# Optimization experiments

Measured on AMD Instinct MI355X. Metric: run time of the kernel, lower is better.

Reference implementation:

```python
import jax, jax.numpy as jnp
import numpy as np

D, H, HD, E, TOPK, F = 2048, 16, 128, 64, 8, 1024
EPS = 1e-5
THETA = 10000.0
ATTN_SCALE = 0.08838834764831845  # 1/sqrt(128)
B, S = 1, 1024


def setup_inputs() -> dict:
    key = jax.random.key(0)
    ks = jax.random.split(key, 16)
    w = 0.02  # init scale so activations stay O(1)
    return {
        "x": jax.random.normal(ks[0], (B, S, D), jnp.float32),
        "input_ln_w": jnp.ones((D,), jnp.float32),
        "q_w": jax.random.normal(ks[1], (D, D), jnp.float32) * w,
        "q_norm_w": jnp.ones((D,), jnp.float32),
        "k_w": jax.random.normal(ks[2], (D, D), jnp.float32) * w,
        "k_norm_w": jnp.ones((D,), jnp.float32),
        "v_w": jax.random.normal(ks[3], (D, D), jnp.float32) * w,
        "o_w": jax.random.normal(ks[4], (D, D), jnp.float32) * w,
        "post_ln_w": jnp.ones((D,), jnp.float32),
        "router_w": jax.random.normal(ks[5], (E, D), jnp.float32) * w,
        "gate_w": jax.random.normal(ks[6], (E, F, D), jnp.float32) * w,
        "up_w": jax.random.normal(ks[7], (E, F, D), jnp.float32) * w,
        "down_w": jax.random.normal(ks[8], (E, D, F), jnp.float32) * w,
    }


def _rmsnorm(h, w):
    return h * jax.lax.rsqrt(jnp.mean(h * h, axis=-1, keepdims=True) + EPS) * w


def _rope(t, cos, sin):
    # t: [B,H,S,HD]; HF rotate_half convention
    t1, t2 = t[..., : HD // 2], t[..., HD // 2 :]
    return jnp.concatenate([t1 * cos - t2 * sin, t2 * cos + t1 * sin], axis=-1)


def reference(x, input_ln_w, q_w, q_norm_w, k_w, k_norm_w, v_w, o_w,
              post_ln_w, router_w, gate_w, up_w, down_w):
    b, s, _ = x.shape
    # ---- attention ----
    xn = _rmsnorm(x, input_ln_w)
    q = _rmsnorm(xn @ q_w.T, q_norm_w)  # full-width q_norm before head split
    k = _rmsnorm(xn @ k_w.T, k_norm_w)
    v = xn @ v_w.T
    q = q.reshape(b, s, H, HD).transpose(0, 2, 1, 3)  # [B,H,S,HD]
    k = k.reshape(b, s, H, HD).transpose(0, 2, 1, 3)
    v = v.reshape(b, s, H, HD).transpose(0, 2, 1, 3)
    pos = jnp.arange(s, dtype=jnp.float32)
    inv_freq = 1.0 / (THETA ** (jnp.arange(0, HD, 2, dtype=jnp.float32) / HD))
    ang = pos[:, None] * inv_freq[None, :]  # [S,HD/2]
    cos, sin = jnp.cos(ang), jnp.sin(ang)
    q, k = _rope(q, cos, sin), _rope(k, cos, sin)
    scores = jnp.einsum("bhqd,bhkd->bhqk", q, k) * ATTN_SCALE
    causal = jnp.tril(jnp.ones((s, s), bool))
    scores = jnp.where(causal, scores, jnp.finfo(scores.dtype).min)
    probs = jax.nn.softmax(scores, axis=-1)
    ctx = jnp.einsum("bhqk,bhkd->bhqd", probs, v)
    attn = ctx.transpose(0, 2, 1, 3).reshape(b, s, D) @ o_w.T
    x = x + attn
    # ---- MoE (top-8 of 64, softmax weights, not renormalized) ----
    h = _rmsnorm(x, post_ln_w)
    logits = h @ router_w.T  # [B,S,E]
    rprobs = jax.nn.softmax(logits.astype(jnp.float32), axis=-1)
    topw, topi = jax.lax.top_k(rprobs, TOPK)  # [B,S,K]
    onehot = jax.nn.one_hot(topi, E, dtype=rprobs.dtype)  # [B,S,K,E]
    wfull = jnp.einsum("bske,bsk->bse", onehot, topw).astype(h.dtype)  # [B,S,E]
    moe = jnp.zeros_like(h)
    for e in range(E):  # fixed expert loop (not a data-dim loop)
        g = h @ gate_w[e].T            # [B,S,F]
        u = h @ up_w[e].T
        y = (jax.nn.silu(g) * u) @ down_w[e].T  # [B,S,D]
        moe = moe + wfull[..., e:e + 1] * y
    return x + moe
```

## Files before the change

### kernel.cpp

```cpp
#include <hip/hip_runtime.h>
#include <hip/hip_bf16.h>
#include <math.h>

#define NTOK 1024
#define DIM 2048
#define NH 16
#define HDIM 128
#define NE 64
#define NTOP 8
#define FF 1024
#define EPSI 1e-5f
#define ASCALE 0.08838834764831845f

typedef __attribute__((ext_vector_type(8))) short bh8;
typedef __attribute__((ext_vector_type(4))) float f4;

static __device__ __forceinline__ ushort f2bf(float f) {
  return __builtin_bit_cast(ushort, __float2bfloat16(f));
}

__global__ __launch_bounds__(256) void k_rmsnorm(const float* __restrict__ in,
                                                 const float* __restrict__ w,
                                                 float* __restrict__ out,
                                                 ushort* __restrict__ outb) {
  int row = blockIdx.x, tid = threadIdx.x;
  const float* r = in + (size_t)row * DIM;
  float ss = 0.f;
  for (int i = tid; i < DIM; i += 256) { float v = r[i]; ss += v * v; }
#pragma unroll
  for (int o = 1; o < 64; o <<= 1) ss += __shfl_xor(ss, o, 64);
  __shared__ float red[4];
  if ((tid & 63) == 0) red[tid >> 6] = ss;
  __syncthreads();
  float rstd = rsqrtf((red[0] + red[1] + red[2] + red[3]) / (float)DIM + EPSI);
  if (out) {
    float* o_ = out + (size_t)row * DIM;
    ushort* ob = outb + (size_t)row * DIM;
    for (int i = tid; i < DIM; i += 256) {
      float v = r[i] * rstd * w[i];
      o_[i] = v; ob[i] = f2bf(v);
    }
  } else {
    ushort* ob = outb + (size_t)row * DIM;
    for (int i = tid; i < DIM; i += 256) ob[i] = f2bf(r[i] * rstd * w[i]);
  }
}

template <int KDIM>
static __device__ __forceinline__ void mm_tile(
    const ushort* __restrict__ Ap0, const ushort* __restrict__ Ap1,
    const float* __restrict__ Wp, ushort (*As)[40], ushort (*Bs)[40],
    int ar0, int ac0, int wrow, int wcol, int wr, int wc, int fr, int fq,
    f4 (&acc)[4][4]) {
  bh8 aR0 = *(const bh8*)Ap0;
  bh8 aR1 = *(const bh8*)Ap1;
  f4 wR[4];
#pragma unroll
  for (int i = 0; i < 4; i++) wR[i] = *(const f4*)(Wp + (size_t)(32 * i) * KDIM);
  for (int k0 = 0; k0 < KDIM; k0 += 32) {
    __syncthreads();
    *(bh8*)&As[ar0][ac0] = aR0;
    *(bh8*)&As[ar0 + 64][ac0] = aR1;
#pragma unroll
    for (int i = 0; i < 4; i++) {
      ushort4 t = make_ushort4(f2bf(wR[i].x), f2bf(wR[i].y), f2bf(wR[i].z), f2bf(wR[i].w));
      *(ushort4*)&Bs[wrow + 32 * i][wcol] = t;
    }
    __syncthreads();
    if (k0 + 32 < KDIM) {
      aR0 = *(const bh8*)(Ap0 + k0 + 32);
      aR1 = *(const bh8*)(Ap1 + k0 + 32);
#pragma unroll
      for (int i = 0; i < 4; i++) wR[i] = *(const f4*)(Wp + (size_t)(32 * i) * KDIM + k0 + 32);
    }
    bh8 af[4], bf_[4];
#pragma unroll
    for (int m = 0; m < 4; m++) af[m] = *(const bh8*)&As[wr * 64 + m * 16 + fr][fq * 8];
#pragma unroll
    for (int n = 0; n < 4; n++) bf_[n] = *(const bh8*)&Bs[wc * 64 + n * 16 + fr][fq * 8];
#pragma unroll
    for (int m = 0; m < 4; m++)
#pragma unroll
      for (int n = 0; n < 4; n++)
        acc[m][n] = __builtin_amdgcn_mfma_f32_16x16x32_bf16(af[m], bf_[n], acc[m][n], 0, 0, 0);
  }
}

__global__ __launch_bounds__(256) void k_gemm_qkv(
    const ushort* __restrict__ A, const float* __restrict__ Wq,
    const float* __restrict__ Wk, const float* __restrict__ Wv,
    float* __restrict__ Cq, float* __restrict__ Ck, float* __restrict__ Cv) {
  __shared__ ushort As[128][40], Bs[128][40];
  int tid = threadIdx.x;
  int m0 = blockIdx.y * 128;
  int ng = blockIdx.x * 128;
  int wsel = ng >> 11, n0 = ng & 2047;
  const float* W = wsel == 0 ? Wq : wsel == 1 ? Wk : Wv;
  float* C = wsel == 0 ? Cq : wsel == 1 ? Ck : Cv;
  int lane = tid & 63, wid = tid >> 6;
  int wr = wid >> 1, wc = wid & 1, fr = lane & 15, fq = lane >> 4;
  int ar0 = tid >> 2, ac0 = (tid & 3) * 8;
  int wrow = tid >> 3, wcol = (tid & 7) * 4;
  const ushort* Ap0 = A + (size_t)(m0 + ar0) * DIM + ac0;
  const ushort* Ap1 = Ap0 + (size_t)64 * DIM;
  const float* Wp = W + (size_t)(n0 + wrow) * DIM + wcol;
  f4 acc[4][4];
  f4 z = {0.f, 0.f, 0.f, 0.f};
#pragma unroll
  for (int m = 0; m < 4; m++)
#pragma unroll
    for (int n = 0; n < 4; n++) acc[m][n] = z;
  mm_tile<DIM>(Ap0, Ap1, Wp, As, Bs, ar0, ac0, wrow, wcol, wr, wc, fr, fq, acc);
#pragma unroll
  for (int m = 0; m < 4; m++)
#pragma unroll
    for (int n = 0; n < 4; n++) {
      int row = m0 + wr * 64 + m * 16 + fq * 4;
      int col = n0 + wc * 64 + n * 16 + fr;
#pragma unroll
      for (int r = 0; r < 4; r++) C[(size_t)(row + r) * DIM + col] = acc[m][n][r];
    }
}

__global__ __launch_bounds__(256) void k_gemm_o(
    const ushort* __restrict__ A, const float* __restrict__ W,
    const float* __restrict__ R, float* __restrict__ C) {
  __shared__ ushort As[128][40], Bs[128][40];
  int tid = threadIdx.x;
  int m0 = blockIdx.y * 128, n0 = blockIdx.x * 128;
  int lane = tid & 63, wid = tid >> 6;
  int wr = wid >> 1, wc = wid & 1, fr = lane & 15, fq = lane >> 4;
  int ar0 = tid >> 2, ac0 = (tid & 3) * 8;
  int wrow = tid >> 3, wcol = (tid & 7) * 4;
  const ushort* Ap0 = A + (size_t)(m0 + ar0) * DIM + ac0;
  const ushort* Ap1 = Ap0 + (size_t)64 * DIM;
  const float* Wp = W + (size_t)(n0 + wrow) * DIM + wcol;
  f4 acc[4][4];
  f4 z = {0.f, 0.f, 0.f, 0.f};
#pragma unroll
  for (int m = 0; m < 4; m++)
#pragma unroll
    for (int n = 0; n < 4; n++) acc[m][n] = z;
  mm_tile<DIM>(Ap0, Ap1, Wp, As, Bs, ar0, ac0, wrow, wcol, wr, wc, fr, fq, acc);
#pragma unroll
  for (int m = 0; m < 4; m++)
#pragma unroll
    for (int n = 0; n < 4; n++) {
      int row = m0 + wr * 64 + m * 16 + fq * 4;
      int col = n0 + wc * 64 + n * 16 + fr;
#pragma unroll
      for (int r = 0; r < 4; r++) {
        size_t o = (size_t)(row + r) * DIM + col;
        C[o] = acc[m][n][r] + R[o];
      }
    }
}

__global__ __launch_bounds__(256) void k_qknorm_rope(
    const float* __restrict__ q, const float* __restrict__ k,
    const float* __restrict__ v, const float* __restrict__ qw,
    const float* __restrict__ kw, float* __restrict__ qr,
    float* __restrict__ kr, float* __restrict__ vr) {
  int s = blockIdx.x, tid = threadIdx.x;
  __shared__ float cst[64], snt[64];
  if (tid < 64) {
    float inv = powf(10000.f, -(float)tid / 64.f);
    float ang = (float)s * inv;
    cst[tid] = cosf(ang);
    snt[tid] = sinf(ang);
  }
  const float* qrow = q + (size_t)s * DIM;
  const float* krow = k + (size_t)s * DIM;
  const float* vrow = v + (size_t)s * DIM;
  float sq = 0.f, sk = 0.f;
  for (int i = tid; i < DIM; i += 256) {
    float a = qrow[i]; sq += a * a;
    float b = krow[i]; sk += b * b;
  }
#pragma unroll
  for (int o = 1; o < 64; o <<= 1) {
    sq += __shfl_xor(sq, o, 64);
    sk += __shfl_xor(sk, o, 64);
  }
  __shared__ float red[8];
  if ((tid & 63) == 0) { red[tid >> 6] = sq; red[4 + (tid >> 6)] = sk; }
  __syncthreads();
  float rq = rsqrtf((red[0] + red[1] + red[2] + red[3]) / (float)DIM + EPSI);
  float rk = rsqrtf((red[4] + red[5] + red[6] + red[7]) / (float)DIM + EPSI);
  for (int idx = tid; idx < NH * 64; idx += 256) {
    int hh = idx >> 6, i = idx & 63;
    float c = cst[i], sn = snt[i];
    int b = hh * HDIM + i;
    float q1 = qrow[b] * rq * qw[b];
    float q2 = qrow[b + 64] * rq * qw[b + 64];
    float k1 = krow[b] * rk * kw[b];
    float k2 = krow[b + 64] * rk * kw[b + 64];
    size_t ob = ((size_t)hh * NTOK + s) * HDIM + i;
    qr[ob] = q1 * c - q2 * sn;
    qr[ob + 64] = q2 * c + q1 * sn;
    kr[ob] = k1 * c - k2 * sn;
    kr[ob + 64] = k2 * c + k1 * sn;
  }
  for (int idx = tid; idx < DIM; idx += 256) {
    int hh = idx >> 7, d = idx & 127;
    vr[((size_t)hh * NTOK + s) * HDIM + d] = vrow[idx];
  }
}

__global__ __launch_bounds__(256) void k_attn(const float* __restrict__ qr,
                                              const float* __restrict__ kr,
                                              const float* __restrict__ vr,
                                              ushort* __restrict__ ctx) {
  int h = blockIdx.y, qt = blockIdx.x;
  __shared__ __align__(16) float Ks[64][HDIM];
  __shared__ __align__(16) float Vs[64][HDIM];
  int tid = threadIdx.x;
  int ql = tid >> 2, sub = tid & 3;
  int qg = qt * 64 + ql;
  const float* qrow = qr + ((size_t)h * NTOK + qg) * HDIM + sub * 32;
  float4 q4[8], acc[8];
#pragma unroll
  for (int i = 0; i < 8; i++) {
    q4[i] = *(const float4*)(qrow + i * 4);
    acc[i] = make_float4(0.f, 0.f, 0.f, 0.f);
  }
  float m = -1e30f, l = 0.f;
  for (int kt = 0; kt <= qt; kt++) {
    __syncthreads();
    const float4* kg = (const float4*)(kr + ((size_t)h * NTOK + kt * 64) * HDIM);
    const float4* vg = (const float4*)(vr + ((size_t)h * NTOK + kt * 64) * HDIM);
#pragma unroll
    for (int i = 0; i < 8; i++) {
      int e4 = tid + i * 256;
      ((float4*)Ks)[e4] = kg[e4];
      ((float4*)Vs)[e4] = vg[e4];
    }
    __syncthreads();
    int jmax = min(64, qg - kt * 64 + 1);
    for (int j = 0; j < jmax; j++) {
      const float4* kj = (const float4*)&Ks[j][sub * 32];
      float sc = 0.f;
#pragma unroll
      for (int i = 0; i < 8; i++) {
        float4 kv = kj[i];
        sc += q4[i].x * kv.x + q4[i].y * kv.y + q4[i].z * kv.z + q4[i].w * kv.w;
      }
      sc += __shfl_xor(sc, 1, 64);
      sc += __shfl_xor(sc, 2, 64);
      sc *= ASCALE;
      float mn = fmaxf(m, sc);
      float al = __expf(m - mn);
      float p = __expf(sc - mn);
      l = l * al + p;
      const float4* vj = (const float4*)&Vs[j][sub * 32];
#pragma unroll
      for (int i = 0; i < 8; i++) {
        float4 vv = vj[i];
        acc[i].x = acc[i].x * al + p * vv.x;
        acc[i].y = acc[i].y * al + p * vv.y;
        acc[i].z = acc[i].z * al + p * vv.z;
        acc[i].w = acc[i].w * al + p * vv.w;
      }
      m = mn;
    }
  }
  float invl = 1.f / l;
  ushort* crow = ctx + (size_t)qg * DIM + h * HDIM + sub * 32;
#pragma unroll
  for (int i = 0; i < 8; i++) {
    float4 o = acc[i];
    ushort4 t = make_ushort4(f2bf(o.x * invl), f2bf(o.y * invl),
                             f2bf(o.z * invl), f2bf(o.w * invl));
    *(ushort4*)(crow + i * 4) = t;
  }
}

__global__ void k_zero_counts(int* counts) {
  if (threadIdx.x < NE) counts[threadIdx.x] = 0;
}

__global__ __launch_bounds__(256) void k_router(const float* __restrict__ h,
                                                const float* __restrict__ rw,
                                                float* __restrict__ topw,
                                                int* __restrict__ lists,
                                                int* __restrict__ counts) {
  int s = blockIdx.x, tid = threadIdx.x;
  int e = tid >> 2, sub = tid & 3;
  const float* hrow = h + (size_t)s * DIM;
  const float* wrow = rw + (size_t)e * DIM;
  float p = 0.f;
  for (int i = sub * 4; i < DIM; i += 16) {
    float4 hv = *(const float4*)(hrow + i);
    float4 wv = *(const float4*)(wrow + i);
    p += hv.x * wv.x + hv.y * wv.y + hv.z * wv.z + hv.w * wv.w;
  }
  p += __shfl_xor(p, 1, 64);
  p += __shfl_xor(p, 2, 64);
  __shared__ float probs[NE];
  if (sub == 0) probs[e] = p;
  __syncthreads();
  if (tid == 0) {
    float mx = -1e30f;
    for (int i = 0; i < NE; i++) mx = fmaxf(mx, probs[i]);
    float sum = 0.f;
    for (int i = 0; i < NE; i++) { probs[i] = __expf(probs[i] - mx); sum += probs[i]; }
    float inv = 1.f / sum;
    for (int kk = 0; kk < NTOP; kk++) {
      float best = -1.f; int bi = 0;
      for (int i = 0; i < NE; i++)
        if (probs[i] > best) { best = probs[i]; bi = i; }
      topw[s * NTOP + kk] = best * inv;
      probs[bi] = -1.f;
      int slot = atomicAdd(&counts[bi], 1);
      lists[bi * NTOK + slot] = s * NTOP + kk;
    }
  }
}

__global__ __launch_bounds__(256) void k_moe_gate_up(
    const ushort* __restrict__ hb, const float* __restrict__ gate,
    const float* __restrict__ up, const int* __restrict__ lists,
    const int* __restrict__ counts, ushort* __restrict__ act) {
  int e = blockIdx.z;
  int nt = counts[e];
  int m0 = blockIdx.y * 128;
  if (m0 >= nt) return;
  __shared__ ushort As[128][40], Gs[128][40], Us[128][40];
  int f0 = blockIdx.x * 128;
  int tid = threadIdx.x;
  int lane = tid & 63, wid = tid >> 6;
  int wr = wid >> 1, wc = wid & 1, fr = lane & 15, fq = lane >> 4;
  int ar0 = tid >> 2, ac0 = (tid & 3) * 8;
  int wrow = tid >> 3, wcol = (tid & 7) * 4;
  int r0 = m0 + ar0, r1 = r0 + 64;
  int g0 = lists[e * NTOK + (r0 < nt ? r0 : nt - 1)];
  int g1 = lists[e * NTOK + (r1 < nt ? r1 : nt - 1)];
  const ushort* Ap0 = hb + (size_t)(g0 >> 3) * DIM + ac0;
  const ushort* Ap1 = hb + (size_t)(g1 >> 3) * DIM + ac0;
  const float* Gp = gate + ((size_t)e * FF + f0 + wrow) * DIM + wcol;
  const float* Up = up + ((size_t)e * FF + f0 + wrow) * DIM + wcol;
  f4 ag[4][4], au[4][4];
  f4 z = {0.f, 0.f, 0.f, 0.f};
#pragma unroll
  for (int m = 0; m < 4; m++)
#pragma unroll
    for (int n = 0; n < 4; n++) { ag[m][n] = z; au[m][n] = z; }
  bh8 aR0 = *(const bh8*)Ap0;
  bh8 aR1 = *(const bh8*)Ap1;
  f4 gR[4], uR[4];
#pragma unroll
  for (int i = 0; i < 4; i++) {
    gR[i] = *(const f4*)(Gp + (size_t)(32 * i) * DIM);
    uR[i] = *(const f4*)(Up + (size_t)(32 * i) * DIM);
  }
  for (int k0 = 0; k0 < DIM; k0 += 32) {
    __syncthreads();
    *(bh8*)&As[ar0][ac0] = aR0;
    *(bh8*)&As[ar0 + 64][ac0] = aR1;
#pragma unroll
    for (int i = 0; i < 4; i++) {
      ushort4 tg = make_ushort4(f2bf(gR[i].x), f2bf(gR[i].y), f2bf(gR[i].z), f2bf(gR[i].w));
      *(ushort4*)&Gs[wrow + 32 * i][wcol] = tg;
      ushort4 tu = make_ushort4(f2bf(uR[i].x), f2bf(uR[i].y), f2bf(uR[i].z), f2bf(uR[i].w));
      *(ushort4*)&Us[wrow + 32 * i][wcol] = tu;
    }
    __syncthreads();
    if (k0 + 32 < DIM) {
      aR0 = *(const bh8*)(Ap0 + k0 + 32);
      aR1 = *(const bh8*)(Ap1 + k0 + 32);
#pragma unroll
      for (int i = 0; i < 4; i++) {
        gR[i] = *(const f4*)(Gp + (size_t)(32 * i) * DIM + k0 + 32);
        uR[i] = *(const f4*)(Up + (size_t)(32 * i) * DIM + k0 + 32);
      }
    }
    bh8 af[4], bg_[4], bu_[4];
#pragma unroll
    for (int m = 0; m < 4; m++) af[m] = *(const bh8*)&As[wr * 64 + m * 16 + fr][fq * 8];
#pragma unroll
    for (int n = 0; n < 4; n++) {
      bg_[n] = *(const bh8*)&Gs[wc * 64 + n * 16 + fr][fq * 8];
      bu_[n] = *(const bh8*)&Us[wc * 64 + n * 16 + fr][fq * 8];
    }
#pragma unroll
    for (int m = 0; m < 4; m++)
#pragma unroll
      for (int n = 0; n < 4; n++) {
        ag[m][n] = __builtin_amdgcn_mfma_f32_16x16x32_bf16(af[m], bg_[n], ag[m][n], 0, 0, 0);
        au[m][n] = __builtin_amdgcn_mfma_f32_16x16x32_bf16(af[m], bu_[n], au[m][n], 0, 0, 0);
      }
  }
#pragma unroll
  for (int m = 0; m < 4; m++) {
#pragma unroll
    for (int r = 0; r < 4; r++) {
      int mrow = m0 + wr * 64 + m * 16 + fq * 4 + r;
      if (mrow < nt) {
        int gg = lists[e * NTOK + mrow];
        ushort* arow = act + (size_t)gg * FF + f0 + wc * 64 + fr;
#pragma unroll
        for (int n = 0; n < 4; n++) {
          float gv = ag[m][n][r], uv = au[m][n][r];
          float sv = gv / (1.f + __expf(-gv)) * uv;
          arow[n * 16] = f2bf(sv);
        }
      }
    }
  }
}

__global__ __launch_bounds__(256) void k_moe_down(
    const ushort* __restrict__ act, const float* __restrict__ down,
    const int* __restrict__ lists, const int* __restrict__ counts,
    const float* __restrict__ topw, float* __restrict__ out) {
  int e = blockIdx.z;
  int nt = counts[e];
  int m0 = blockIdx.y * 128;
  if (m0 >= nt) return;
  __shared__ ushort As[128][40], Bs[128][40];
  int n0 = blockIdx.x * 128;
  int tid = threadIdx.x;
  int lane = tid & 63, wid = tid >> 6;
  int wr = wid >> 1, wc = wid & 1, fr = lane & 15, fq = lane >> 4;
  int ar0 = tid >> 2, ac0 = (tid & 3) * 8;
  int wrow = tid >> 3, wcol = (tid & 7) * 4;
  int r0 = m0 + ar0, r1 = r0 + 64;
  int g0 = lists[e * NTOK + (r0 < nt ? r0 : nt - 1)];
  int g1 = lists[e * NTOK + (r1 < nt ? r1 : nt - 1)];
  const ushort* Ap0 = act + (size_t)g0 * FF + ac0;
  const ushort* Ap1 = act + (size_t)g1 * FF + ac0;
  const float* Wp = down + ((size_t)e * DIM + n0 + wrow) * FF + wcol;
  f4 acc[4][4];
  f4 z = {0.f, 0.f, 0.f, 0.f};
#pragma unroll
  for (int m = 0; m < 4; m++)
#pragma unroll
    for (int n = 0; n < 4; n++) acc[m][n] = z;
  mm_tile<FF>(Ap0, Ap1, Wp, As, Bs, ar0, ac0, wrow, wcol, wr, wc, fr, fq, acc);
#pragma unroll
  for (int m = 0; m < 4; m++) {
#pragma unroll
    for (int r = 0; r < 4; r++) {
      int mrow = m0 + wr * 64 + m * 16 + fq * 4 + r;
      if (mrow < nt) {
        int gg = lists[e * NTOK + mrow];
        int s = gg >> 3;
        float wgt = topw[gg];
        float* orow = out + (size_t)s * DIM + n0 + wc * 64 + fr;
#pragma unroll
        for (int n = 0; n < 4; n++) atomicAdd(&orow[n * 16], wgt * acc[m][n][r]);
      }
    }
  }
}

extern "C" void kernel_launch(void* const* d_in, const int* in_sizes, int n_in,
                              void* d_out, int out_size, void* d_ws, size_t ws_size,
                              hipStream_t stream) {
  const float* x   = (const float*)d_in[0];
  const float* iln = (const float*)d_in[1];
  const float* qw  = (const float*)d_in[2];
  const float* qnw = (const float*)d_in[3];
  const float* kw  = (const float*)d_in[4];
  const float* knw = (const float*)d_in[5];
  const float* vw  = (const float*)d_in[6];
  const float* ow  = (const float*)d_in[7];
  const float* pln = (const float*)d_in[8];
  const float* rw  = (const float*)d_in[9];
  const float* gw  = (const float*)d_in[10];
  const float* uw  = (const float*)d_in[11];
  const float* dw  = (const float*)d_in[12];
  float* out = (float*)d_out;
  float* ws = (float*)d_ws;

  const size_t M2 = (size_t)NTOK * DIM;
  float* qb = ws + 0 * M2;
  float* kb = ws + 1 * M2;
  float* vb = ws + 2 * M2;
  float* qr = ws + 3 * M2;
  float* kr = ws + 4 * M2;
  float* vr = ws + 5 * M2;
  ushort* xnb = (ushort*)(ws + 6 * M2);
  ushort* hb  = xnb + M2;
  ushort* ctxb = (ushort*)kb;
  float* topw = kb + M2 / 2;
  int* lists = (int*)(topw + NTOK * NTOP);
  int* counts = lists + NE * NTOK;
  float* h = qb;
  ushort* act = (ushort*)vb;

  k_rmsnorm<<<NTOK, 256, 0, stream>>>(x, iln, nullptr, xnb);
  k_gemm_qkv<<<dim3(48, 8), 256, 0, stream>>>(xnb, qw, kw, vw, qb, kb, vb);
  k_qknorm_rope<<<NTOK, 256, 0, stream>>>(qb, kb, vb, qnw, knw, qr, kr, vr);
  k_attn<<<dim3(NTOK / 64, NH), 256, 0, stream>>>(qr, kr, vr, ctxb);
  k_gemm_o<<<dim3(16, 8), 256, 0, stream>>>(ctxb, ow, x, out);
  k_rmsnorm<<<NTOK, 256, 0, stream>>>(out, pln, h, hb);
  k_zero_counts<<<1, 64, 0, stream>>>(counts);
  k_router<<<NTOK, 256, 0, stream>>>(h, rw, topw, lists, counts);
  k_moe_gate_up<<<dim3(FF / 128, NTOK / 128, NE), 256, 0, stream>>>(hb, gw, uw, lists, counts, act);
  k_moe_down<<<dim3(DIM / 128, NTOK / 128, NE), 256, 0, stream>>>(act, dw, lists, counts, topw, out);
}
```

Baseline: 2.489 ms.

## Rewrite MoE expert GEMMs as LDS-free register-direct MFMA with expert-fastest block ordering

The MoE gate/up and down kernels no longer stage tiles in shared memory and no longer synchronise. Each wave now loads its 16-row weight slice straight from global memory, converts it to bf16 in registers, and runs MFMA against 8 gathered token rows. The tile shrinks to 128 tokens by 64 outputs. The grid becomes 1-D with the expert index varying fastest, so active experts spread across CUs and early-exit blocks interleave. This removes the LDS traffic and barriers, but activation rows are re-read from global/L2 by every wave and each thread issues narrow scattered stores and atomics.

```diff
diff --git a/kernel.cpp b/kernel.cpp
--- a/kernel.cpp
+++ b/kernel.cpp
@@ -17,6 +17,15 @@
 
 static __device__ __forceinline__ ushort f2bf(float f) {
   return __builtin_bit_cast(ushort, __float2bfloat16(f));
+}
+
+static __device__ __forceinline__ bh8 packbf(f4 lo, f4 hi) {
+  bh8 r;
+  r[0] = (short)f2bf(lo[0]); r[1] = (short)f2bf(lo[1]);
+  r[2] = (short)f2bf(lo[2]); r[3] = (short)f2bf(lo[3]);
+  r[4] = (short)f2bf(hi[0]); r[5] = (short)f2bf(hi[1]);
+  r[6] = (short)f2bf(hi[2]); r[7] = (short)f2bf(hi[3]);
+  return r;
 }
 
 __global__ __launch_bounds__(256) void k_rmsnorm(const float* __restrict__ in,
@@ -321,89 +330,65 @@
     const ushort* __restrict__ hb, const float* __restrict__ gate,
     const float* __restrict__ up, const int* __restrict__ lists,
     const int* __restrict__ counts, ushort* __restrict__ act) {
-  int e = blockIdx.z;
+  int gid = blockIdx.x;
+  int e = gid & 63, fb = (gid >> 6) & 15, mb = gid >> 10;
   int nt = counts[e];
-  int m0 = blockIdx.y * 128;
+  int m0 = mb * 128;
   if (m0 >= nt) return;
-  __shared__ ushort As[128][40], Gs[128][40], Us[128][40];
-  int f0 = blockIdx.x * 128;
   int tid = threadIdx.x;
-  int lane = tid & 63, wid = tid >> 6;
-  int wr = wid >> 1, wc = wid & 1, fr = lane & 15, fq = lane >> 4;
-  int ar0 = tid >> 2, ac0 = (tid & 3) * 8;
-  int wrow = tid >> 3, wcol = (tid & 7) * 4;
-  int r0 = m0 + ar0, r1 = r0 + 64;
-  int g0 = lists[e * NTOK + (r0 < nt ? r0 : nt - 1)];
-  int g1 = lists[e * NTOK + (r1 < nt ? r1 : nt - 1)];
-  const ushort* Ap0 = hb + (size_t)(g0 >> 3) * DIM + ac0;
-  const ushort* Ap1 = hb + (size_t)(g1 >> 3) * DIM + ac0;
-  const float* Gp = gate + ((size_t)e * FF + f0 + wrow) * DIM + wcol;
-  const float* Up = up + ((size_t)e * FF + f0 + wrow) * DIM + wcol;
-  f4 ag[4][4], au[4][4];
+  int lane = tid & 63, w = tid >> 6;
+  int fr = lane & 15, fq = lane >> 4;
+  int frow = fb * 64 + w * 16 + fr;
+  const float* gp = gate + ((size_t)e * FF + frow) * DIM + fq * 8;
+  const float* pp = up + ((size_t)e * FF + frow) * DIM + fq * 8;
+  const ushort* ap[8];
+#pragma unroll
+  for (int m = 0; m < 8; m++) {
+    int mr = m0 + m * 16 + fr;
+    int g = lists[e * NTOK + (mr < nt ? mr : nt - 1)];
+    ap[m] = hb + (size_t)(g >> 3) * DIM + fq * 8;
+  }
+  f4 accg[8], accu[8];
   f4 z = {0.f, 0.f, 0.f, 0.f};
 #pragma unroll
-  for (int m = 0; m < 4; m++)
-#pragma unroll
-    for (int n = 0; n < 4; n++) { ag[m][n] = z; au[m][n] = z; }
-  bh8 aR0 = *(const bh8*)Ap0;
-  bh8 aR1 = *(const bh8*)Ap1;
-  f4 gR[4], uR[4];
-#pragma unroll
-  for (int i = 0; i < 4; i++) {
-    gR[i] = *(const f4*)(Gp + (size_t)(32 * i) * DIM);
-    uR[i] = *(const f4*)(Up + (size_t)(32 * i) * DIM);
-  }
-  for (int k0 = 0; k0 < DIM; k0 += 32) {
-    __syncthreads();
-    *(bh8*)&As[ar0][ac0] = aR0;
-    *(bh8*)&As[ar0 + 64][ac0] = aR1;
-#pragma unroll
-    for (int i = 0; i < 4; i++) {
-      ushort4 tg = make_ushort4(f2bf(gR[i].x), f2bf(gR[i].y), f2bf(gR[i].z), f2bf(gR[i].w));
-      *(ushort4*)&Gs[wrow + 32 * i][wcol] = tg;
-      ushort4 tu = make_ushort4(f2bf(uR[i].x), f2bf(uR[i].y), f2bf(uR[i].z), f2bf(uR[i].w));
-      *(ushort4*)&Us[wrow + 32 * i][wcol] = tu;
-    }
-    __syncthreads();
-    if (k0 + 32 < DIM) {
-      aR0 = *(const bh8*)(Ap0 + k0 + 32);
-      aR1 = *(const bh8*)(Ap1 + k0 + 32);
-#pragma unroll
-      for (int i = 0; i < 4; i++) {
-        gR[i] = *(const f4*)(Gp + (size_t)(32 * i) * DIM + k0 + 32);
-        uR[i] = *(const f4*)(Up + (size_t)(32 * i) * DIM + k0 + 32);
-      }
-    }
-    bh8 af[4], bg_[4], bu_[4];
-#pragma unroll
-    for (int m = 0; m < 4; m++) af[m] = *(const bh8*)&As[wr * 64 + m * 16 + fr][fq * 8];
-#pragma unroll
-    for (int n = 0; n < 4; n++) {
-      bg_[n] = *(const bh8*)&Gs[wc * 64 + n * 16 + fr][fq * 8];
-      bu_[n] = *(const bh8*)&Us[wc * 64 + n * 16 + fr][fq * 8];
-    }
-#pragma unroll
-    for (int m = 0; m < 4; m++)
-#pragma unroll
-      for (int n = 0; n < 4; n++) {
-        ag[m][n] = __builtin_amdgcn_mfma_f32_16x16x32_bf16(af[m], bg_[n], ag[m][n], 0, 0, 0);
-        au[m][n] = __builtin_amdgcn_mfma_f32_16x16x32_bf16(af[m], bu_[n], au[m][n], 0, 0, 0);
-      }
-  }
-#pragma unroll
-  for (int m = 0; m < 4; m++) {
+  for (int m = 0; m < 8; m++) { accg[m] = z; accu[m] = z; }
+  f4 g0 = *(const f4*)gp, g1 = *(const f4*)(gp + 4);
+  f4 u0 = *(const f4*)pp, u1 = *(const f4*)(pp + 4);
+  int k0 = 0;
+  for (; k0 < DIM - 32; k0 += 32) {
+    f4 ng0 = *(const f4*)(gp + k0 + 32), ng1 = *(const f4*)(gp + k0 + 36);
+    f4 nu0 = *(const f4*)(pp + k0 + 32), nu1 = *(const f4*)(pp + k0 + 36);
+    bh8 a[8];
+#pragma unroll
+    for (int m = 0; m < 8; m++) a[m] = *(const bh8*)(ap[m] + k0);
+    bh8 bg = packbf(g0, g1), bu = packbf(u0, u1);
+#pragma unroll
+    for (int m = 0; m < 8; m++) {
+      accg[m] = __builtin_amdgcn_mfma_f32_16x16x32_bf16(a[m], bg, accg[m], 0, 0, 0);
+      accu[m] = __builtin_amdgcn_mfma_f32_16x16x32_bf16(a[m], bu, accu[m], 0, 0, 0);
+    }
+    g0 = ng0; g1 = ng1; u0 = nu0; u1 = nu1;
+  }
+  {
+    bh8 a[8];
+#pragma unroll
+    for (int m = 0; m < 8; m++) a[m] = *(const bh8*)(ap[m] + k0);
+    bh8 bg = packbf(g0, g1), bu = packbf(u0, u1);
+#pragma unroll
+    for (int m = 0; m < 8; m++) {
+      accg[m] = __builtin_amdgcn_mfma_f32_16x16x32_bf16(a[m], bg, accg[m], 0, 0, 0);
+      accu[m] = __builtin_amdgcn_mfma_f32_16x16x32_bf16(a[m], bu, accu[m], 0, 0, 0);
+    }
+  }
+#pragma unroll
+  for (int m = 0; m < 8; m++) {
 #pragma unroll
     for (int r = 0; r < 4; r++) {
-      int mrow = m0 + wr * 64 + m * 16 + fq * 4 + r;
+      int mrow = m0 + m * 16 + fq * 4 + r;
       if (mrow < nt) {
         int gg = lists[e * NTOK + mrow];
-        ushort* arow = act + (size_t)gg * FF + f0 + wc * 64 + fr;
-#pragma unroll
-        for (int n = 0; n < 4; n++) {
-          float gv = ag[m][n][r], uv = au[m][n][r];
-          float sv = gv / (1.f + __expf(-gv)) * uv;
-          arow[n * 16] = f2bf(sv);
-        }
+        float gv = accg[m][r], uv = accu[m][r];
+        act[(size_t)gg * FF + frow] = f2bf(gv / (1.f + __expf(-gv)) * uv);
       }
     }
   }
@@ -413,42 +398,57 @@
     const ushort* __restrict__ act, const float* __restrict__ down,
     const int* __restrict__ lists, const int* __restrict__ counts,
     const float* __restrict__ topw, float* __restrict__ out) {
-  int e = blockIdx.z;
+  int gid = blockIdx.x;
+  int e = gid & 63, nb = (gid >> 6) & 31, mb = gid >> 11;
   int nt = counts[e];
-  int m0 = blockIdx.y * 128;
+  int m0 = mb * 128;
   if (m0 >= nt) return;
-  __shared__ ushort As[128][40], Bs[128][40];
-  int n0 = blockIdx.x * 128;
   int tid = threadIdx.x;
-  int lane = tid & 63, wid = tid >> 6;
-  int wr = wid >> 1, wc = wid & 1, fr = lane & 15, fq = lane >> 4;
-  int ar0 = tid >> 2, ac0 = (tid & 3) * 8;
-  int wrow = tid >> 3, wcol = (tid & 7) * 4;
-  int r0 = m0 + ar0, r1 = r0 + 64;
-  int g0 = lists[e * NTOK + (r0 < nt ? r0 : nt - 1)];
-  int g1 = lists[e * NTOK + (r1 < nt ? r1 : nt - 1)];
-  const ushort* Ap0 = act + (size_t)g0 * FF + ac0;
-  const ushort* Ap1 = act + (size_t)g1 * FF + ac0;
-  const float* Wp = down + ((size_t)e * DIM + n0 + wrow) * FF + wcol;
-  f4 acc[4][4];
+  int lane = tid & 63, w = tid >> 6;
+  int fr = lane & 15, fq = lane >> 4;
+  int nrow = nb * 64 + w * 16 + fr;
+  const float* wp = down + ((size_t)e * DIM + nrow) * FF + fq * 8;
+  const ushort* ap[8];
+#pragma unroll
+  for (int m = 0; m < 8; m++) {
+    int mr = m0 + m * 16 + fr;
+    int g = lists[e * NTOK + (mr < nt ? mr : nt - 1)];
+    ap[m] = act + (size_t)g * FF + fq * 8;
+  }
+  f4 acc[8];
   f4 z = {0.f, 0.f, 0.f, 0.f};
 #pragma unroll
-  for (int m = 0; m < 4; m++)
-#pragma unroll
-    for (int n = 0; n < 4; n++) acc[m][n] = z;
-  mm_tile<FF>(Ap0, Ap1, Wp, As, Bs, ar0, ac0, wrow, wcol, wr, wc, fr, fq, acc);
-#pragma unroll
-  for (int m = 0; m < 4; m++) {
+  for (int m = 0; m < 8; m++) acc[m] = z;
+  f4 b0 = *(const f4*)wp, b1 = *(const f4*)(wp + 4);
+  int k0 = 0;
+  for (; k0 < FF - 32; k0 += 32) {
+    f4 nb0 = *(const f4*)(wp + k0 + 32), nb1 = *(const f4*)(wp + k0 + 36);
+    bh8 a[8];
+#pragma unroll
+    for (int m = 0; m < 8; m++) a[m] = *(const bh8*)(ap[m] + k0);
+    bh8 bb = packbf(b0, b1);
+#pragma unroll
+    for (int m = 0; m < 8; m++)
+      acc[m] = __builtin_amdgcn_mfma_f32_16x16x32_bf16(a[m], bb, acc[m], 0, 0, 0);
+    b0 = nb0; b1 = nb1;
+  }
+  {
+    bh8 a[8];
+#pragma unroll
+    for (int m = 0; m < 8; m++) a[m] = *(const bh8*)(ap[m] + k0);
+    bh8 bb = packbf(b0, b1);
+#pragma unroll
+    for (int m = 0; m < 8; m++)
+      acc[m] = __builtin_amdgcn_mfma_f32_16x16x32_bf16(a[m], bb, acc[m], 0, 0, 0);
+  }
+#pragma unroll
+  for (int m = 0; m < 8; m++) {
 #pragma unroll
     for (int r = 0; r < 4; r++) {
-      int mrow = m0 + wr * 64 + m * 16 + fq * 4 + r;
+      int mrow = m0 + m * 16 + fq * 4 + r;
       if (mrow < nt) {
         int gg = lists[e * NTOK + mrow];
-        int s = gg >> 3;
-        float wgt = topw[gg];
-        float* orow = out + (size_t)s * DIM + n0 + wc * 64 + fr;
-#pragma unroll
-        for (int n = 0; n < 4; n++) atomicAdd(&orow[n * 16], wgt * acc[m][n][r]);
+        atomicAdd(&out[(size_t)(gg >> 3) * DIM + nrow], topw[gg] * acc[m][r]);
       }
     }
   }
@@ -497,6 +497,6 @@
   k_rmsnorm<<<NTOK, 256, 0, stream>>>(out, pln, h, hb);
   k_zero_counts<<<1, 64, 0, stream>>>(counts);
   k_router<<<NTOK, 256, 0, stream>>>(h, rw, topw, lists, counts);
-  k_moe_gate_up<<<dim3(FF / 128, NTOK / 128, NE), 256, 0, stream>>>(hb, gw, uw, lists, counts, act);
-  k_moe_down<<<dim3(DIM / 128, NTOK / 128, NE), 256, 0, stream>>>(act, dw, lists, counts, topw, out);
-}
+  k_moe_gate_up<<<8192, 256, 0, stream>>>(hb, gw, uw, lists, counts, act);
+  k_moe_down<<<16384, 256, 0, stream>>>(act, dw, lists, counts, topw, out);
+}
```

Measured after the change: 2.827 ms. +13.6%, slower.
